# Kernel tuning notes

Hardware: AMD Instinct MI355X
Metric: run time of the kernel (lower is better)

Reference implementation:

```python
import jax, jax.numpy as jnp
import numpy as np

N = 100000
E = 3200000
H = 32
L = 2
LN_EPS = 1e-5


def _layer_norm(x, g, b):
    mu = jnp.mean(x, axis=-1, keepdims=True)
    var = jnp.mean(jnp.square(x - mu), axis=-1, keepdims=True)
    return (x - mu) * jax.lax.rsqrt(var + LN_EPS) * g + b


def setup_inputs() -> dict:
    key = jax.random.key(0)
    ks = jax.random.split(key, 32)
    aa_idx = jax.random.randint(ks[0], (N,), 0, 21)
    atom_idx = jax.random.randint(ks[1], (N,), 0, 3)
    edge_index = jax.random.randint(ks[2], (2, E), 0, N)
    edge_attr = jax.random.uniform(ks[3], (E, 4), dtype=jnp.float32)
    edge_attr = edge_attr.at[:, 0].multiply(30.0)  # distances in [0, 30)
    s = 0.1
    p = {
        'aa_emb': jax.random.normal(ks[4], (21, 16), jnp.float32) * s,
        'atom_emb': jax.random.normal(ks[5], (3, 16), jnp.float32) * s,
        'proj_W1': jax.random.normal(ks[6], (32, H), jnp.float32) * s,
        'proj_b1': jnp.zeros((H,), jnp.float32),
        'proj_W2': jax.random.normal(ks[7], (H, H), jnp.float32) * s,
        'proj_b2': jnp.zeros((H,), jnp.float32),
        'short_eps': jnp.zeros((L,), jnp.float32),
        'short_eW': jax.random.normal(ks[8], (L, 4, H), jnp.float32) * s,
        'short_eb': jnp.zeros((L, H), jnp.float32),
        'short_W1': jax.random.normal(ks[9], (L, H, H), jnp.float32) * s,
        'short_b1': jnp.zeros((L, H), jnp.float32),
        'short_W2': jax.random.normal(ks[10], (L, H, H), jnp.float32) * s,
        'short_b2': jnp.zeros((L, H), jnp.float32),
        'long_eps': jnp.zeros((L,), jnp.float32),
        'long_eW': jax.random.normal(ks[11], (L, 4, H), jnp.float32) * s,
        'long_eb': jnp.zeros((L, H), jnp.float32),
        'long_W1': jax.random.normal(ks[12], (L, H, H), jnp.float32) * s,
        'long_b1': jnp.zeros((L, H), jnp.float32),
        'long_W2': jax.random.normal(ks[13], (L, H, H), jnp.float32) * s,
        'long_b2': jnp.zeros((L, H), jnp.float32),
        'ln_g': jnp.ones((L, H), jnp.float32),
        'ln_b': jnp.zeros((L, H), jnp.float32),
        'head_W1': jax.random.normal(ks[14], (H, 16), jnp.float32) * s,
        'head_b1': jnp.zeros((16,), jnp.float32),
        'head_W2': jax.random.normal(ks[15], (16, 8), jnp.float32) * s,
        'head_b2': jnp.zeros((8,), jnp.float32),
        'head_W3': jax.random.normal(ks[16], (8, 8), jnp.float32) * s,
        'head_b3': jnp.zeros((8,), jnp.float32),
    }
    return dict(aa_idx=aa_idx, atom_idx=atom_idx, edge_index=edge_index, edge_attr=edge_attr, **p)


def _gine(h, edge_attr, src, dst, mask, eps, eW, eb, W1, b1, W2, b2):
    # GINEConv: msg = relu(x_src + lin(edge_attr)); sum into dst; nn((1+eps)*x + aggr)
    msg = jax.nn.relu(h[src] + edge_attr @ eW + eb) * mask[:, None]
    aggr = jax.ops.segment_sum(msg, dst, num_segments=h.shape[0])
    z = (1.0 + eps) * h + aggr
    return jax.nn.relu(z @ W1 + b1) @ W2 + b2


def reference(aa_idx, atom_idx, edge_index, edge_attr,
              aa_emb, atom_emb, proj_W1, proj_b1, proj_W2, proj_b2,
              short_eps, short_eW, short_eb, short_W1, short_b1, short_W2, short_b2,
              long_eps, long_eW, long_eb, long_W1, long_b1, long_W2, long_b2,
              ln_g, ln_b, head_W1, head_b1, head_W2, head_b2, head_W3, head_b3):
    x = jnp.concatenate([aa_emb[aa_idx], atom_emb[atom_idx]], axis=-1)  # [N, 32]
    h = jax.nn.relu(x @ proj_W1 + proj_b1) @ proj_W2 + proj_b2  # [N, H]

    dist = edge_attr[:, 0]
    src, dst = edge_index[0], edge_index[1]
    ca = (atom_idx == 1)
    short_mask = ((dist >= 0.0) & (dist < 10.0)).astype(h.dtype)
    long_mask = ((dist >= 0.0) & (dist <= 25.0) & ca[src] & ca[dst]).astype(h.dtype)

    for l in range(L):
        h_s = _gine(h, edge_attr, src, dst, short_mask, short_eps[l], short_eW[l], short_eb[l], short_W1[l], short_b1[l], short_W2[l], short_b2[l])
        h_l = _gine(h, edge_attr, src, dst, long_mask, long_eps[l], long_eW[l], long_eb[l], long_W1[l], long_b1[l], long_W2[l], long_b2[l])
        h = _layer_norm(h + h_s + h_l, ln_g[l], ln_b[l])
        h = jax.nn.relu(h)  # dropout is identity in eval mode

    h = jax.nn.relu(h @ head_W1 + head_b1)
    h = jax.nn.relu(h @ head_W2 + head_b2)
    return h @ head_W3 + head_b3  # [N, 8]
```

## Files before the change

### kernel.cpp

```cpp
#include <hip/hip_runtime.h>

#define NN 100000
#define NE 3200000
#define CAP 1500000
#define NBUCK 391
#define BK_CAP 4096
#define PP_EPT 4
#define PP_BS 1024
#define NBLK ((NE + PP_BS * PP_EPT - 1) / (PP_BS * PP_EPT))
#define NW ((NN + 31) / 32)

typedef unsigned long long u64;
typedef unsigned int u32;


__device__ __forceinline__ void mv32(const float* __restrict__ W,
                                     const float* __restrict__ b,
                                     const float* __restrict__ x,
                                     float* __restrict__ o, bool do_relu) {
#pragma unroll
  for (int c = 0; c < 32; ++c) o[c] = b[c];
#pragma unroll
  for (int k = 0; k < 32; ++k) {
    float xk = x[k];
#pragma unroll
    for (int c = 0; c < 32; ++c) o[c] = fmaf(xk, W[k * 32 + c], o[c]);
  }
  if (do_relu) {
#pragma unroll
    for (int c = 0; c < 32; ++c) o[c] = fmaxf(o[c], 0.f);
  }
}

__global__ __launch_bounds__(256) void k_ca(
    const int* __restrict__ atom_idx, u32* __restrict__ caBits) {
  int w = blockIdx.x * 256 + threadIdx.x;
  if (w >= NW) return;
  int base = w * 32;
  int lim = NN - base; if (lim > 32) lim = 32;
  u32 bits = 0;
  for (int j = 0; j < lim; ++j)
    bits |= (atom_idx[base + j] == 1 ? 1u : 0u) << j;
  caBits[w] = bits;
}

__global__ __launch_bounds__(256) void k_init(
    const int* __restrict__ aa_idx, const int* __restrict__ atom_idx,
    const float* __restrict__ aa_emb, const float* __restrict__ atom_emb,
    const float* __restrict__ W1, const float* __restrict__ b1,
    const float* __restrict__ W2, const float* __restrict__ b2,
    float* __restrict__ h) {
  __shared__ float sW1[1024], sW2[1024], sb1[32], sb2[32];
  int t = threadIdx.x;
  for (int i = t; i < 1024; i += 256) { sW1[i] = W1[i]; sW2[i] = W2[i]; }
  if (t < 32) { sb1[t] = b1[t]; sb2[t] = b2[t]; }
  __syncthreads();
  int n = blockIdx.x * 256 + t;
  if (n >= NN) return;
  int aa = aa_idx[n], at = atom_idx[n];
  float x[32];
  const float4* ar = (const float4*)(aa_emb + aa * 16);
  const float4* trp = (const float4*)(atom_emb + at * 16);
#pragma unroll
  for (int q = 0; q < 4; ++q) {
    float4 v = ar[q];
    x[q*4+0]=v.x; x[q*4+1]=v.y; x[q*4+2]=v.z; x[q*4+3]=v.w;
  }
#pragma unroll
  for (int q = 0; q < 4; ++q) {
    float4 v = trp[q];
    x[16+q*4+0]=v.x; x[16+q*4+1]=v.y; x[16+q*4+2]=v.z; x[16+q*4+3]=v.w;
  }
  float tmp[32], o[32];
  mv32(sW1, sb1, x, tmp, true);
  mv32(sW2, sb2, tmp, o, false);
  float4* hrow = (float4*)(h + (size_t)n * 32);
#pragma unroll
  for (int q = 0; q < 8; ++q)
    hrow[q] = make_float4(o[q*4], o[q*4+1], o[q*4+2], o[q*4+3]);
}

__global__ __launch_bounds__(PP_BS) void k_preprocess(
    const int* __restrict__ edge_index, const float4* __restrict__ edge_attr,
    const u32* __restrict__ caBits,
    uint4* __restrict__ elist, int* __restrict__ cnt,
    int* __restrict__ hist, int* __restrict__ segStart, int* __restrict__ segCnt) {
  __shared__ int swc[PP_BS / 64];
  __shared__ int sbase;
  __shared__ int lhist[NBUCK];
  __shared__ u32 lcab[NW];
  int t = threadIdx.x;
  for (int i = t; i < NBUCK; i += PP_BS) lhist[i] = 0;
  for (int i = t; i < NW; i += PP_BS) lcab[i] = caBits[i];
  __syncthreads();
  int lane = t & 63, wid = t >> 6;
  int base = blockIdx.x * (PP_BS * PP_EPT) + t;
  uint4 ent[PP_EPT];
  unsigned mbs[PP_EPT];
  int pre[PP_EPT];
  int wtot = 0;
#pragma unroll
  for (int q = 0; q < PP_EPT; ++q) {
    int e = base + q * PP_BS;
    unsigned mb = 0;
    uint4 en = make_uint4(0, 0, 0, 0);
    if (e < NE) {
      float4 a = edge_attr[e];
      float dist = a.x;
      if (dist >= 0.f && dist <= 25.f) {
        int s = edge_index[e];
        int d = edge_index[NE + e];
        unsigned sb = (dist < 10.f) ? 1u : 0u;
        u32 cs = (lcab[(u32)s >> 5] >> (s & 31)) & 1u;
        u32 cd = (lcab[(u32)d >> 5] >> (d & 31)) & 1u;
        unsigned lb = (cs & cd) << 1;
        mb = sb | lb;
        if (mb) {
          u32 cat = (mb == 1u) ? 0u : ((mb == 3u) ? 1u : 2u);
          u32 qx = (u32)(dist * (65535.f / 25.f) + 0.5f);
          u32 qy = (u32)(a.y * 65535.f + 0.5f);
          u32 qz = (u32)(a.z * 65535.f + 0.5f);
          u32 qw = (u32)(a.w * 65535.f + 0.5f);
          en.x = (u32)s | (cat << 17);
          en.y = (u32)d;
          en.z = qx | (qy << 16);
          en.w = qz | (qw << 16);
          atomicAdd(&lhist[d >> 8], 1);
        }
      }
    }
    ent[q] = en; mbs[q] = mb;
    unsigned long long bal = __ballot(mb != 0);
    pre[q] = wtot + __popcll(bal & ((1ull << lane) - 1ull));
    wtot += (int)__popcll(bal);
  }
  if (lane == 0) swc[wid] = wtot;
  __syncthreads();
  if (t == 0) {
    int tot = 0;
#pragma unroll
    for (int w = 0; w < PP_BS / 64; ++w) { int c = swc[w]; swc[w] = tot; tot += c; }
    sbase = atomicAdd(cnt, tot);
    segStart[blockIdx.x] = sbase;
    segCnt[blockIdx.x] = tot;
  }
  __syncthreads();
  int mybase = sbase + swc[wid];
#pragma unroll
  for (int q = 0; q < PP_EPT; ++q)
    if (mbs[q]) elist[mybase + pre[q]] = ent[q];
  for (int i = t; i < NBUCK; i += PP_BS)
    hist[(size_t)blockIdx.x * NBUCK + i] = lhist[i];
}

__global__ __launch_bounds__(1024) void kA(
    const int* __restrict__ hist, int* __restrict__ cpT, int* __restrict__ bucketTotal) {
  __shared__ int s[1024];
  int b = blockIdx.x;
  int t = threadIdx.x;
  int v = (t < NBLK) ? hist[(size_t)t * NBUCK + b] : 0;
  s[t] = v;
  __syncthreads();
  for (int off = 1; off < 1024; off <<= 1) {
    int a = (t >= off) ? s[t - off] : 0;
    __syncthreads();
    s[t] += a;
    __syncthreads();
  }
  if (t < NBLK) cpT[(size_t)t * NBUCK + b] = s[t] - v;
  if (t == NBLK - 1) bucketTotal[b] = s[t];
}

__global__ __launch_bounds__(512) void kB(
    const int* __restrict__ bucketTotal, int* __restrict__ bucketBase,
    int* __restrict__ row_ptr) {
  __shared__ int sc[512];
  int t = threadIdx.x;
  int v0 = (t < NBUCK) ? bucketTotal[t] : 0;
  sc[t] = v0;
  __syncthreads();
  for (int off = 1; off < 512; off <<= 1) {
    int a = (t >= off) ? sc[t - off] : 0;
    __syncthreads();
    sc[t] += a;
    __syncthreads();
  }
  int incl = sc[t];
  if (t < NBUCK) bucketBase[t] = incl - v0;
  if (t == NBUCK - 1) { bucketBase[NBUCK] = incl; row_ptr[NN] = incl; }
}

__global__ __launch_bounds__(256) void k_place(
    const uint4* __restrict__ elist, const int* __restrict__ segStart,
    const int* __restrict__ segCnt, const int* __restrict__ bucketBase,
    const int* __restrict__ cpT, uint4* __restrict__ part) {
  __shared__ int baseB[NBUCK];
  __shared__ int cur[NBUCK];
  int k = blockIdx.x;
  int t = threadIdx.x;
  for (int b = t; b < NBUCK; b += 256) {
    baseB[b] = bucketBase[b] + cpT[(size_t)k * NBUCK + b];
    cur[b] = 0;
  }
  __syncthreads();
  int s0 = segStart[k], n0 = segCnt[k];
  for (int i = t; i < n0; i += 256) {
    uint4 en = elist[s0 + i];
    int b = (int)(en.y >> 8);
    int r = atomicAdd(&cur[b], 1);
    part[baseB[b] + r] = en;
  }
}

__global__ __launch_bounds__(1024) void k_sort(
    const uint4* __restrict__ part, const int* __restrict__ bucketBase,
    uint4* __restrict__ rec, int* __restrict__ row_ptr) {
  __shared__ uint4 sbuf[BK_CAP];
  __shared__ int hist[768], cur[768];
  __shared__ int wpart[4];
  int b = blockIdx.x;
  int t = threadIdx.x;
  int base = bucketBase[b];
  int cntB = bucketBase[b + 1] - base;
  if (cntB > BK_CAP) cntB = BK_CAP;
  if (t < 768) hist[t] = 0;
  __syncthreads();
  for (int i = t; i < cntB; i += 1024) {
    uint4 en = part[base + i];
    sbuf[i] = en;
    int bin = (int)(en.y & 255u) * 3 + (int)(en.x >> 17);
    atomicAdd(&hist[bin], 1);
  }
  __syncthreads();
  int h0 = 0, h1 = 0, s0 = 0, inc = 0;
  int lane = t & 63;
  if (t < 256) {
    h0 = hist[3 * t]; h1 = hist[3 * t + 1];
    int h2 = hist[3 * t + 2];
    s0 = h0 + h1 + h2;
    inc = s0;
#pragma unroll
    for (int d = 1; d < 64; d <<= 1) {
      int o = __shfl_up(inc, d);
      if (lane >= d) inc += o;
    }
    if (lane == 63) wpart[t >> 6] = inc;
  }
  __syncthreads();
  if (t < 256) {
    int woff = 0;
#pragma unroll
    for (int w = 0; w < 4; ++w)
      if (w < (t >> 6)) woff += wpart[w];
    int ex = woff + inc - s0;
    cur[3 * t] = ex; cur[3 * t + 1] = ex + h0; cur[3 * t + 2] = ex + h0 + h1;
    int node = b * 256 + t;
    if (node < NN) row_ptr[node] = base + ex;
  }
  __syncthreads();
  for (int i = t; i < cntB; i += 1024) {
    uint4 en = sbuf[i];
    int bin = (int)(en.y & 255u) * 3 + (int)(en.x >> 17);
    int r = atomicAdd(&cur[bin], 1);
    rec[base + r] = en;
  }
}

#define AG_BLOCKS 4096
__device__ __forceinline__ void accum_edge(
    uint4 r, int c, const float* __restrict__ h,
    float ws0, float ws1, float ws2, float ws3, float bs,
    float wl0, float wl1, float wl2, float wl3, float bl,
    float& acc_s, float& acc_l) {
  int s = (int)(r.x & 0x1FFFFu);
  u32 cat = r.x >> 17;
  float hv = h[(size_t)s * 32 + c];
  float ax = (float)(r.z & 0xFFFFu);
  float ay = (float)(r.z >> 16);
  float az = (float)(r.w & 0xFFFFu);
  float aw = (float)(r.w >> 16);
  float ts = bs + ax * ws0 + ay * ws1 + az * ws2 + aw * ws3;
  float tl = bl + ax * wl0 + ay * wl1 + az * wl2 + aw * wl3;
  float ms = (cat <= 1u) ? 1.f : 0.f;
  float ml = (cat >= 1u) ? 1.f : 0.f;
  acc_s = fmaf(ms, fmaxf(hv + ts, 0.f), acc_s);
  acc_l = fmaf(ml, fmaxf(hv + tl, 0.f), acc_l);
}

__global__ __launch_bounds__(256) void k_aggr(
    const int* __restrict__ row_ptr, const uint4* __restrict__ rec,
    const float* __restrict__ h,
    float* __restrict__ aggr_s, float* __restrict__ aggr_l,
    const float* __restrict__ eW_s, const float* __restrict__ eb_s,
    const float* __restrict__ eW_l, const float* __restrict__ eb_l) {
  int t = threadIdx.x;
  int lane = t & 63;
  int c = lane & 31;
  int half = lane >> 5;
  int wave = (blockIdx.x * 256 + t) >> 6;
  int nwaves = (gridDim.x * 256) >> 6;
  const float qd = 25.f / 65535.f, q1 = 1.f / 65535.f;
  float ws0 = eW_s[c] * qd, ws1 = eW_s[32 + c] * q1,
        ws2 = eW_s[64 + c] * q1, ws3 = eW_s[96 + c] * q1;
  float bs = eb_s[c];
  float wl0 = eW_l[c] * qd, wl1 = eW_l[32 + c] * q1,
        wl2 = eW_l[64 + c] * q1, wl3 = eW_l[96 + c] * q1;
  float bl = eb_l[c];
  for (int node = wave; node < NN; node += nwaves) {
    int start = row_ptr[node];
    int end = row_ptr[node + 1];
    float acc_s = 0.f, acc_l = 0.f;
    int i = start + half;
    for (; i + 2 < end; i += 4) {
      uint4 r0 = rec[i];
      uint4 r1 = rec[i + 2];
      accum_edge(r0, c, h, ws0, ws1, ws2, ws3, bs, wl0, wl1, wl2, wl3, bl, acc_s, acc_l);
      accum_edge(r1, c, h, ws0, ws1, ws2, ws3, bs, wl0, wl1, wl2, wl3, bl, acc_s, acc_l);
    }
    if (i < end) {
      uint4 r0 = rec[i];
      accum_edge(r0, c, h, ws0, ws1, ws2, ws3, bs, wl0, wl1, wl2, wl3, bl, acc_s, acc_l);
    }
    float rs = acc_s + __shfl_xor(acc_s, 32);
    float rl = acc_l + __shfl_xor(acc_l, 32);
    if (half == 0) aggr_s[(size_t)node * 32 + c] = rs;
    else           aggr_l[(size_t)node * 32 + c] = rl;
  }
}

template <bool LAST>
__global__ __launch_bounds__(256) void k_node(
    float* __restrict__ h, const float* __restrict__ aggr_s, const float* __restrict__ aggr_l,
    const float* __restrict__ eps_s, const float* __restrict__ eps_l,
    const float* __restrict__ W1s, const float* __restrict__ b1s,
    const float* __restrict__ W2s, const float* __restrict__ b2s,
    const float* __restrict__ W1l, const float* __restrict__ b1l,
    const float* __restrict__ W2l, const float* __restrict__ b2l,
    const float* __restrict__ lng, const float* __restrict__ lnb,
    const float* __restrict__ hW1, const float* __restrict__ hb1,
    const float* __restrict__ hW2, const float* __restrict__ hb2,
    const float* __restrict__ hW3, const float* __restrict__ hb3,
    float* __restrict__ out) {
  __shared__ float sW1s[1024], sW2s[1024], sW1l[1024], sW2l[1024];
  __shared__ float sb1s[32], sb2s[32], sb1l[32], sb2l[32], sg[32], sbn[32];
  __shared__ float sh1[512], sh2[128], sh3[64], shb1[16], shb2[8], shb3[8];
  int t = threadIdx.x;
  for (int i = t; i < 1024; i += 256) {
    sW1s[i] = W1s[i]; sW2s[i] = W2s[i]; sW1l[i] = W1l[i]; sW2l[i] = W2l[i];
  }
  if (t < 32) {
    sb1s[t] = b1s[t]; sb2s[t] = b2s[t]; sb1l[t] = b1l[t]; sb2l[t] = b2l[t];
    sg[t] = lng[t]; sbn[t] = lnb[t];
  }
  if (LAST) {
    for (int i = t; i < 512; i += 256) sh1[i] = hW1[i];
    if (t < 128) sh2[t] = hW2[t];
    if (t < 64) sh3[t] = hW3[t];
    if (t < 16) shb1[t] = hb1[t];
    if (t < 8) { shb2[t] = hb2[t]; shb3[t] = hb3[t]; }
  }
  __syncthreads();
  float es = 1.f + eps_s[0];
  float el = 1.f + eps_l[0];
  int n = blockIdx.x * 256 + t;
  if (n >= NN) return;
  float4* hrow = (float4*)(h + (size_t)n * 32);
  const float4* asr = (const float4*)(aggr_s + (size_t)n * 32);
  const float4* alr = (const float4*)(aggr_l + (size_t)n * 32);
  float hv[32], x[32], z[32], tt[32];
#pragma unroll
  for (int q = 0; q < 8; ++q) {
    float4 v = hrow[q];
    hv[q*4+0]=v.x; hv[q*4+1]=v.y; hv[q*4+2]=v.z; hv[q*4+3]=v.w;
  }
#pragma unroll
  for (int q = 0; q < 8; ++q) {
    float4 v = asr[q];
    z[q*4+0]=v.x; z[q*4+1]=v.y; z[q*4+2]=v.z; z[q*4+3]=v.w;
  }
#pragma unroll
  for (int c = 0; c < 32; ++c) z[c] = fmaf(es, hv[c], z[c]);
  mv32(sW1s, sb1s, z, tt, true);
  mv32(sW2s, sb2s, tt, x, false);
#pragma unroll
  for (int c = 0; c < 32; ++c) x[c] += hv[c];
#pragma unroll
  for (int q = 0; q < 8; ++q) {
    float4 v = alr[q];
    z[q*4+0]=v.x; z[q*4+1]=v.y; z[q*4+2]=v.z; z[q*4+3]=v.w;
  }
#pragma unroll
  for (int c = 0; c < 32; ++c) z[c] = fmaf(el, hv[c], z[c]);
  mv32(sW1l, sb1l, z, tt, true);
  mv32(sW2l, sb2l, tt, hv, false);
#pragma unroll
  for (int c = 0; c < 32; ++c) x[c] += hv[c];
  float mu = 0.f;
#pragma unroll
  for (int c = 0; c < 32; ++c) mu += x[c];
  mu *= (1.f / 32.f);
  float var = 0.f;
#pragma unroll
  for (int c = 0; c < 32; ++c) { float dd = x[c] - mu; var += dd * dd; }
  var *= (1.f / 32.f);
  float rs = rsqrtf(var + 1e-5f);
#pragma unroll
  for (int c = 0; c < 32; ++c) {
    float y = (x[c] - mu) * rs * sg[c] + sbn[c];
    x[c] = fmaxf(y, 0.f);
  }
  if (!LAST) {
#pragma unroll
    for (int q = 0; q < 8; ++q)
      hrow[q] = make_float4(x[q*4], x[q*4+1], x[q*4+2], x[q*4+3]);
  } else {
    float t16[16];
#pragma unroll
    for (int j = 0; j < 16; ++j) t16[j] = shb1[j];
#pragma unroll
    for (int k = 0; k < 32; ++k) {
      float xk = x[k];
#pragma unroll
      for (int j = 0; j < 16; ++j) t16[j] = fmaf(xk, sh1[k * 16 + j], t16[j]);
    }
#pragma unroll
    for (int j = 0; j < 16; ++j) t16[j] = fmaxf(t16[j], 0.f);
    float t8[8];
#pragma unroll
    for (int j = 0; j < 8; ++j) t8[j] = shb2[j];
#pragma unroll
    for (int k = 0; k < 16; ++k) {
      float xk = t16[k];
#pragma unroll
      for (int j = 0; j < 8; ++j) t8[j] = fmaf(xk, sh2[k * 8 + j], t8[j]);
    }
#pragma unroll
    for (int j = 0; j < 8; ++j) t8[j] = fmaxf(t8[j], 0.f);
    float o8[8];
#pragma unroll
    for (int j = 0; j < 8; ++j) o8[j] = shb3[j];
#pragma unroll
    for (int k = 0; k < 8; ++k) {
      float xk = t8[k];
#pragma unroll
      for (int j = 0; j < 8; ++j) o8[j] = fmaf(xk, sh3[k * 8 + j], o8[j]);
    }
    float4* orow = (float4*)(out + (size_t)n * 8);
    orow[0] = make_float4(o8[0], o8[1], o8[2], o8[3]);
    orow[1] = make_float4(o8[4], o8[5], o8[6], o8[7]);
  }
}

extern "C" void kernel_launch(void* const* d_in, const int* in_sizes, int n_in,
                              void* d_out, int out_size, void* d_ws, size_t ws_size,
                              hipStream_t stream) {
  const int*   aa_idx     = (const int*)d_in[0];
  const int*   atom_idx   = (const int*)d_in[1];
  const int*   edge_index = (const int*)d_in[2];
  const float* edge_attr  = (const float*)d_in[3];
  const float* aa_emb     = (const float*)d_in[4];
  const float* atom_emb   = (const float*)d_in[5];
  const float* proj_W1    = (const float*)d_in[6];
  const float* proj_b1    = (const float*)d_in[7];
  const float* proj_W2    = (const float*)d_in[8];
  const float* proj_b2    = (const float*)d_in[9];
  const float* short_eps  = (const float*)d_in[10];
  const float* short_eW   = (const float*)d_in[11];
  const float* short_eb   = (const float*)d_in[12];
  const float* short_W1   = (const float*)d_in[13];
  const float* short_b1   = (const float*)d_in[14];
  const float* short_W2   = (const float*)d_in[15];
  const float* short_b2   = (const float*)d_in[16];
  const float* long_eps   = (const float*)d_in[17];
  const float* long_eW    = (const float*)d_in[18];
  const float* long_eb    = (const float*)d_in[19];
  const float* long_W1    = (const float*)d_in[20];
  const float* long_b1    = (const float*)d_in[21];
  const float* long_W2    = (const float*)d_in[22];
  const float* long_b2    = (const float*)d_in[23];
  const float* ln_g       = (const float*)d_in[24];
  const float* ln_b       = (const float*)d_in[25];
  const float* head_W1    = (const float*)d_in[26];
  const float* head_b1    = (const float*)d_in[27];
  const float* head_W2    = (const float*)d_in[28];
  const float* head_b2    = (const float*)d_in[29];
  const float* head_W3    = (const float*)d_in[30];
  const float* head_b3    = (const float*)d_in[31];
  float* out = (float*)d_out;

  char* p = (char*)d_ws;
  uint4* rec     = (uint4*)p;                 p += (size_t)CAP * 16;
  uint4* elist   = (uint4*)p;                 p += (size_t)CAP * 16;
  float* h       = (float*)p;                 p += (size_t)NN * 32 * 4;
  float* aggr_s  = (float*)p;                 p += (size_t)NN * 32 * 4;
  float* aggr_l  = (float*)p;                 p += (size_t)NN * 32 * 4;
  int*   row_ptr = (int*)p;                   p += (size_t)(NN + 1) * 4;
  int*   hist    = (int*)p;                   p += (size_t)NBLK * NBUCK * 4;
  int*   cpT     = (int*)p;                   p += (size_t)NBLK * NBUCK * 4;
  int*   segStart= (int*)p;                   p += (size_t)NBLK * 4;
  int*   segCnt  = (int*)p;                   p += (size_t)NBLK * 4;
  int*   bucketBase = (int*)p;                p += (size_t)(NBUCK + 1) * 4;
  int*   bucketTotal= (int*)p;                p += (size_t)NBUCK * 4;
  u32*   caBits  = (u32*)p;                   p += (size_t)NW * 4;
  int*   cnt     = (int*)p;
  uint4* part    = (uint4*)aggr_s;

  hipMemsetAsync(cnt, 0, sizeof(int), stream);

  k_ca<<<(NW + 255) / 256, 256, 0, stream>>>(atom_idx, caBits);

  k_init<<<(NN + 255) / 256, 256, 0, stream>>>(
      aa_idx, atom_idx, aa_emb, atom_emb, proj_W1, proj_b1, proj_W2, proj_b2, h);

  k_preprocess<<<NBLK, PP_BS, 0, stream>>>(
      edge_index, (const float4*)edge_attr, caBits, elist, cnt,
      hist, segStart, segCnt);

  kA<<<NBUCK, 1024, 0, stream>>>(hist, cpT, bucketTotal);
  kB<<<1, 512, 0, stream>>>(bucketTotal, bucketBase, row_ptr);

  k_place<<<NBLK, 256, 0, stream>>>(
      elist, segStart, segCnt, bucketBase, cpT, part);

  k_sort<<<NBUCK, 1024, 0, stream>>>(part, bucketBase, rec, row_ptr);

  for (int l = 0; l < 2; ++l) {
    k_aggr<<<AG_BLOCKS, 256, 0, stream>>>(
        row_ptr, rec, h, aggr_s, aggr_l,
        short_eW + l * 128, short_eb + l * 32, long_eW + l * 128, long_eb + l * 32);
    if (l == 0) {
      k_node<false><<<(NN + 255) / 256, 256, 0, stream>>>(
          h, aggr_s, aggr_l, short_eps + l, long_eps + l,
          short_W1 + l * 1024, short_b1 + l * 32, short_W2 + l * 1024, short_b2 + l * 32,
          long_W1 + l * 1024, long_b1 + l * 32, long_W2 + l * 1024, long_b2 + l * 32,
          ln_g + l * 32, ln_b + l * 32,
          nullptr, nullptr, nullptr, nullptr, nullptr, nullptr, out);
    } else {
      k_node<true><<<(NN + 255) / 256, 256, 0, stream>>>(
          h, aggr_s, aggr_l, short_eps + l, long_eps + l,
          short_W1 + l * 1024, short_b1 + l * 32, short_W2 + l * 1024, short_b2 + l * 32,
          long_W1 + l * 1024, long_b1 + l * 32, long_W2 + l * 1024, long_b2 + l * 32,
          ln_g + l * 32, ln_b + l * 32,
          head_W1, head_b1, head_W2, head_b2, head_W3, head_b3, out);
    }
  }
}
```

Before: 277.7 us.

## Replace per-node CSR sort with 32-node buckets and LDS atomic aggregation

Shrinks the bucket width from 256 to 32 destination nodes and drops the per-bucket counting-sort kernel and row_ptr. The aggregation kernel now processes a whole bucket per block and accumulates edge messages into shared-memory tiles with float atomics before writing them out. Histogram and prefix offsets are stored as 16-bit values in a single reused buffer, and the bucket-base scan is reorganised for 3125 buckets. This removes a full sort pass and its global traffic, at the cost of LDS atomic contention and nondeterministic float summation order.

```diff
diff --git a/kernel.cpp b/kernel.cpp
--- a/kernel.cpp
+++ b/kernel.cpp
@@ -3,8 +3,8 @@
 #define NN 100000
 #define NE 3200000
 #define CAP 1500000
-#define NBUCK 391
-#define BK_CAP 4096
+#define BSH 5
+#define NBUCK 3125
 #define PP_EPT 4
 #define PP_BS 1024
 #define NBLK ((NE + PP_BS * PP_EPT - 1) / (PP_BS * PP_EPT))
@@ -12,6 +12,7 @@
 
 typedef unsigned long long u64;
 typedef unsigned int u32;
+typedef unsigned short u16;
 
 
 __device__ __forceinline__ void mv32(const float* __restrict__ W,
@@ -84,7 +85,7 @@
     const int* __restrict__ edge_index, const float4* __restrict__ edge_attr,
     const u32* __restrict__ caBits,
     uint4* __restrict__ elist, int* __restrict__ cnt,
-    int* __restrict__ hist, int* __restrict__ segStart, int* __restrict__ segCnt) {
+    u16* __restrict__ hist, int* __restrict__ segStart, int* __restrict__ segCnt) {
   __shared__ int swc[PP_BS / 64];
   __shared__ int sbase;
   __shared__ int lhist[NBUCK];
@@ -125,7 +126,7 @@
           en.y = (u32)d;
           en.z = qx | (qy << 16);
           en.w = qz | (qw << 16);
-          atomicAdd(&lhist[d >> 8], 1);
+          atomicAdd(&lhist[d >> BSH], 1);
         }
       }
     }
@@ -150,15 +151,15 @@
   for (int q = 0; q < PP_EPT; ++q)
     if (mbs[q]) elist[mybase + pre[q]] = ent[q];
   for (int i = t; i < NBUCK; i += PP_BS)
-    hist[(size_t)blockIdx.x * NBUCK + i] = lhist[i];
+    hist[(size_t)blockIdx.x * NBUCK + i] = (u16)lhist[i];
 }
 
 __global__ __launch_bounds__(1024) void kA(
-    const int* __restrict__ hist, int* __restrict__ cpT, int* __restrict__ bucketTotal) {
+    u16* __restrict__ hist, int* __restrict__ bucketTotal) {
   __shared__ int s[1024];
   int b = blockIdx.x;
   int t = threadIdx.x;
-  int v = (t < NBLK) ? hist[(size_t)t * NBUCK + b] : 0;
+  int v = (t < NBLK) ? (int)hist[(size_t)t * NBUCK + b] : 0;
   s[t] = v;
   __syncthreads();
   for (int off = 1; off < 1024; off <<= 1) {
@@ -167,138 +168,99 @@
     s[t] += a;
     __syncthreads();
   }
-  if (t < NBLK) cpT[(size_t)t * NBUCK + b] = s[t] - v;
+  if (t < NBLK) hist[(size_t)t * NBUCK + b] = (u16)(s[t] - v);
   if (t == NBLK - 1) bucketTotal[b] = s[t];
 }
 
-__global__ __launch_bounds__(512) void kB(
-    const int* __restrict__ bucketTotal, int* __restrict__ bucketBase,
-    int* __restrict__ row_ptr) {
-  __shared__ int sc[512];
-  int t = threadIdx.x;
-  int v0 = (t < NBUCK) ? bucketTotal[t] : 0;
-  sc[t] = v0;
-  __syncthreads();
-  for (int off = 1; off < 512; off <<= 1) {
-    int a = (t >= off) ? sc[t - off] : 0;
-    __syncthreads();
-    sc[t] += a;
-    __syncthreads();
-  }
-  int incl = sc[t];
-  if (t < NBUCK) bucketBase[t] = incl - v0;
-  if (t == NBUCK - 1) { bucketBase[NBUCK] = incl; row_ptr[NN] = incl; }
+__global__ __launch_bounds__(1024) void kB(
+    const int* __restrict__ bucketTotal, int* __restrict__ bucketBase) {
+  __shared__ int ws2[16];
+  int t = threadIdx.x;
+  int lane = t & 63, wid = t >> 6;
+  int i0 = t * 4;
+  int v[4];
+  int s = 0;
+#pragma unroll
+  for (int q = 0; q < 4; ++q) {
+    int x = (i0 + q < NBUCK) ? bucketTotal[i0 + q] : 0;
+    v[q] = s; s += x;
+  }
+  int inc = s;
+#pragma unroll
+  for (int d = 1; d < 64; d <<= 1) {
+    int o = __shfl_up(inc, d);
+    if (lane >= d) inc += o;
+  }
+  if (lane == 63) ws2[wid] = inc;
+  __syncthreads();
+  int woff = 0;
+#pragma unroll
+  for (int w = 0; w < 16; ++w)
+    if (w < wid) woff += ws2[w];
+  int ex = woff + inc - s;
+#pragma unroll
+  for (int q = 0; q < 4; ++q) {
+    int i = i0 + q;
+    if (i < NBUCK) bucketBase[i] = ex + v[q];
+  }
+  if (t == 1023) {
+    int tot = 0;
+#pragma unroll
+    for (int w = 0; w < 16; ++w) tot += ws2[w];
+    bucketBase[NBUCK] = tot;
+  }
 }
 
 __global__ __launch_bounds__(256) void k_place(
     const uint4* __restrict__ elist, const int* __restrict__ segStart,
     const int* __restrict__ segCnt, const int* __restrict__ bucketBase,
-    const int* __restrict__ cpT, uint4* __restrict__ part) {
+    const u16* __restrict__ cpT, uint4* __restrict__ part) {
   __shared__ int baseB[NBUCK];
   __shared__ int cur[NBUCK];
   int k = blockIdx.x;
   int t = threadIdx.x;
   for (int b = t; b < NBUCK; b += 256) {
-    baseB[b] = bucketBase[b] + cpT[(size_t)k * NBUCK + b];
+    baseB[b] = bucketBase[b] + (int)cpT[(size_t)k * NBUCK + b];
     cur[b] = 0;
   }
   __syncthreads();
   int s0 = segStart[k], n0 = segCnt[k];
   for (int i = t; i < n0; i += 256) {
     uint4 en = elist[s0 + i];
-    int b = (int)(en.y >> 8);
+    int b = (int)(en.y >> BSH);
     int r = atomicAdd(&cur[b], 1);
     part[baseB[b] + r] = en;
   }
 }
 
-__global__ __launch_bounds__(1024) void k_sort(
-    const uint4* __restrict__ part, const int* __restrict__ bucketBase,
-    uint4* __restrict__ rec, int* __restrict__ row_ptr) {
-  __shared__ uint4 sbuf[BK_CAP];
-  __shared__ int hist[768], cur[768];
-  __shared__ int wpart[4];
-  int b = blockIdx.x;
-  int t = threadIdx.x;
-  int base = bucketBase[b];
-  int cntB = bucketBase[b + 1] - base;
-  if (cntB > BK_CAP) cntB = BK_CAP;
-  if (t < 768) hist[t] = 0;
-  __syncthreads();
-  for (int i = t; i < cntB; i += 1024) {
-    uint4 en = part[base + i];
-    sbuf[i] = en;
-    int bin = (int)(en.y & 255u) * 3 + (int)(en.x >> 17);
-    atomicAdd(&hist[bin], 1);
-  }
-  __syncthreads();
-  int h0 = 0, h1 = 0, s0 = 0, inc = 0;
-  int lane = t & 63;
-  if (t < 256) {
-    h0 = hist[3 * t]; h1 = hist[3 * t + 1];
-    int h2 = hist[3 * t + 2];
-    s0 = h0 + h1 + h2;
-    inc = s0;
-#pragma unroll
-    for (int d = 1; d < 64; d <<= 1) {
-      int o = __shfl_up(inc, d);
-      if (lane >= d) inc += o;
-    }
-    if (lane == 63) wpart[t >> 6] = inc;
-  }
-  __syncthreads();
-  if (t < 256) {
-    int woff = 0;
-#pragma unroll
-    for (int w = 0; w < 4; ++w)
-      if (w < (t >> 6)) woff += wpart[w];
-    int ex = woff + inc - s0;
-    cur[3 * t] = ex; cur[3 * t + 1] = ex + h0; cur[3 * t + 2] = ex + h0 + h1;
-    int node = b * 256 + t;
-    if (node < NN) row_ptr[node] = base + ex;
-  }
-  __syncthreads();
-  for (int i = t; i < cntB; i += 1024) {
-    uint4 en = sbuf[i];
-    int bin = (int)(en.y & 255u) * 3 + (int)(en.x >> 17);
-    int r = atomicAdd(&cur[bin], 1);
-    rec[base + r] = en;
-  }
-}
-
-#define AG_BLOCKS 4096
-__device__ __forceinline__ void accum_edge(
-    uint4 r, int c, const float* __restrict__ h,
+#define AGB_BLOCKS 512
+__device__ __forceinline__ void agg_edge(
+    uint4 en, float hv, int c,
     float ws0, float ws1, float ws2, float ws3, float bs,
     float wl0, float wl1, float wl2, float wl3, float bl,
-    float& acc_s, float& acc_l) {
-  int s = (int)(r.x & 0x1FFFFu);
-  u32 cat = r.x >> 17;
-  float hv = h[(size_t)s * 32 + c];
-  float ax = (float)(r.z & 0xFFFFu);
-  float ay = (float)(r.z >> 16);
-  float az = (float)(r.w & 0xFFFFu);
-  float aw = (float)(r.w >> 16);
-  float ts = bs + ax * ws0 + ay * ws1 + az * ws2 + aw * ws3;
-  float tl = bl + ax * wl0 + ay * wl1 + az * wl2 + aw * wl3;
-  float ms = (cat <= 1u) ? 1.f : 0.f;
-  float ml = (cat >= 1u) ? 1.f : 0.f;
-  acc_s = fmaf(ms, fmaxf(hv + ts, 0.f), acc_s);
-  acc_l = fmaf(ml, fmaxf(hv + tl, 0.f), acc_l);
-}
-
-__global__ __launch_bounds__(256) void k_aggr(
-    const int* __restrict__ row_ptr, const uint4* __restrict__ rec,
+    float* __restrict__ lds_s, float* __restrict__ lds_l) {
+  u32 cat = (en.x >> 17) & 3u;
+  int dl = (int)(en.y & 31u);
+  float ax = (float)(en.z & 0xFFFFu), ay = (float)(en.z >> 16);
+  float az = (float)(en.w & 0xFFFFu), aw = (float)(en.w >> 16);
+  float bsx = (cat <= 1u) ? bs : -1e30f;
+  float blx = (cat >= 1u) ? bl : -1e30f;
+  float ts = fmaf(ax, ws0, fmaf(ay, ws1, fmaf(az, ws2, fmaf(aw, ws3, bsx))));
+  float tl = fmaf(ax, wl0, fmaf(ay, wl1, fmaf(az, wl2, fmaf(aw, wl3, blx))));
+  atomicAdd(&lds_s[dl * 32 + c], fmaxf(hv + ts, 0.f));
+  atomicAdd(&lds_l[dl * 32 + c], fmaxf(hv + tl, 0.f));
+}
+
+__global__ __launch_bounds__(1024) void k_aggrB(
+    const int* __restrict__ bucketBase, const uint4* __restrict__ part,
     const float* __restrict__ h,
     float* __restrict__ aggr_s, float* __restrict__ aggr_l,
     const float* __restrict__ eW_s, const float* __restrict__ eb_s,
     const float* __restrict__ eW_l, const float* __restrict__ eb_l) {
-  int t = threadIdx.x;
-  int lane = t & 63;
-  int c = lane & 31;
-  int half = lane >> 5;
-  int wave = (blockIdx.x * 256 + t) >> 6;
-  int nwaves = (gridDim.x * 256) >> 6;
+  __shared__ float lds_s[1024], lds_l[1024];
+  int t = threadIdx.x;
+  int c = t & 31;
+  int grp = t >> 5;
   const float qd = 25.f / 65535.f, q1 = 1.f / 65535.f;
   float ws0 = eW_s[c] * qd, ws1 = eW_s[32 + c] * q1,
         ws2 = eW_s[64 + c] * q1, ws3 = eW_s[96 + c] * q1;
@@ -306,25 +268,28 @@
   float wl0 = eW_l[c] * qd, wl1 = eW_l[32 + c] * q1,
         wl2 = eW_l[64 + c] * q1, wl3 = eW_l[96 + c] * q1;
   float bl = eb_l[c];
-  for (int node = wave; node < NN; node += nwaves) {
-    int start = row_ptr[node];
-    int end = row_ptr[node + 1];
-    float acc_s = 0.f, acc_l = 0.f;
-    int i = start + half;
-    for (; i + 2 < end; i += 4) {
-      uint4 r0 = rec[i];
-      uint4 r1 = rec[i + 2];
-      accum_edge(r0, c, h, ws0, ws1, ws2, ws3, bs, wl0, wl1, wl2, wl3, bl, acc_s, acc_l);
-      accum_edge(r1, c, h, ws0, ws1, ws2, ws3, bs, wl0, wl1, wl2, wl3, bl, acc_s, acc_l);
-    }
-    if (i < end) {
-      uint4 r0 = rec[i];
-      accum_edge(r0, c, h, ws0, ws1, ws2, ws3, bs, wl0, wl1, wl2, wl3, bl, acc_s, acc_l);
-    }
-    float rs = acc_s + __shfl_xor(acc_s, 32);
-    float rl = acc_l + __shfl_xor(acc_l, 32);
-    if (half == 0) aggr_s[(size_t)node * 32 + c] = rs;
-    else           aggr_l[(size_t)node * 32 + c] = rl;
+  for (int b = blockIdx.x; b < NBUCK; b += AGB_BLOCKS) {
+    lds_s[t] = 0.f; lds_l[t] = 0.f;
+    __syncthreads();
+    int s0 = bucketBase[b], e0 = bucketBase[b + 1];
+    int i = s0 + grp;
+    for (; i + 32 < e0; i += 64) {
+      uint4 en0 = part[i];
+      uint4 en1 = part[i + 32];
+      float hv0 = h[(size_t)(en0.x & 0x1FFFFu) * 32 + c];
+      float hv1 = h[(size_t)(en1.x & 0x1FFFFu) * 32 + c];
+      agg_edge(en0, hv0, c, ws0, ws1, ws2, ws3, bs, wl0, wl1, wl2, wl3, bl, lds_s, lds_l);
+      agg_edge(en1, hv1, c, ws0, ws1, ws2, ws3, bs, wl0, wl1, wl2, wl3, bl, lds_s, lds_l);
+    }
+    if (i < e0) {
+      uint4 en0 = part[i];
+      float hv0 = h[(size_t)(en0.x & 0x1FFFFu) * 32 + c];
+      agg_edge(en0, hv0, c, ws0, ws1, ws2, ws3, bs, wl0, wl1, wl2, wl3, bl, lds_s, lds_l);
+    }
+    __syncthreads();
+    aggr_s[(size_t)b * 1024 + t] = lds_s[t];
+    aggr_l[(size_t)b * 1024 + t] = lds_l[t];
+    __syncthreads();
   }
 }
 
@@ -489,21 +454,18 @@
   float* out = (float*)d_out;
 
   char* p = (char*)d_ws;
-  uint4* rec     = (uint4*)p;                 p += (size_t)CAP * 16;
   uint4* elist   = (uint4*)p;                 p += (size_t)CAP * 16;
+  uint4* part    = (uint4*)p;                 p += (size_t)CAP * 16;
   float* h       = (float*)p;                 p += (size_t)NN * 32 * 4;
   float* aggr_s  = (float*)p;                 p += (size_t)NN * 32 * 4;
   float* aggr_l  = (float*)p;                 p += (size_t)NN * 32 * 4;
-  int*   row_ptr = (int*)p;                   p += (size_t)(NN + 1) * 4;
-  int*   hist    = (int*)p;                   p += (size_t)NBLK * NBUCK * 4;
-  int*   cpT     = (int*)p;                   p += (size_t)NBLK * NBUCK * 4;
+  u16*   hist    = (u16*)p;                   p += (size_t)NBLK * NBUCK * 2;
   int*   segStart= (int*)p;                   p += (size_t)NBLK * 4;
   int*   segCnt  = (int*)p;                   p += (size_t)NBLK * 4;
   int*   bucketBase = (int*)p;                p += (size_t)(NBUCK + 1) * 4;
   int*   bucketTotal= (int*)p;                p += (size_t)NBUCK * 4;
   u32*   caBits  = (u32*)p;                   p += (size_t)NW * 4;
   int*   cnt     = (int*)p;
-  uint4* part    = (uint4*)aggr_s;
 
   hipMemsetAsync(cnt, 0, sizeof(int), stream);
 
@@ -516,17 +478,15 @@
       edge_index, (const float4*)edge_attr, caBits, elist, cnt,
       hist, segStart, segCnt);
 
-  kA<<<NBUCK, 1024, 0, stream>>>(hist, cpT, bucketTotal);
-  kB<<<1, 512, 0, stream>>>(bucketTotal, bucketBase, row_ptr);
+  kA<<<NBUCK, 1024, 0, stream>>>(hist, bucketTotal);
+  kB<<<1, 1024, 0, stream>>>(bucketTotal, bucketBase);
 
   k_place<<<NBLK, 256, 0, stream>>>(
-      elist, segStart, segCnt, bucketBase, cpT, part);
-
-  k_sort<<<NBUCK, 1024, 0, stream>>>(part, bucketBase, rec, row_ptr);
+      elist, segStart, segCnt, bucketBase, hist, part);
 
   for (int l = 0; l < 2; ++l) {
-    k_aggr<<<AG_BLOCKS, 256, 0, stream>>>(
-        row_ptr, rec, h, aggr_s, aggr_l,
+    k_aggrB<<<AGB_BLOCKS, 1024, 0, stream>>>(
+        bucketBase, part, h, aggr_s, aggr_l,
         short_eW + l * 128, short_eb + l * 32, long_eW + l * 128, long_eb + l * 32);
     if (l == 0) {
       k_node<false><<<(NN + 255) / 256, 256, 0, stream>>>(
```

Result: slower. 1.063 ms (+283.0%).
